# Kernel tuning notes

Hardware: AMD Instinct MI355X
Metric: run time of the kernel (lower is better)

The kernel has to match this reference:

```python
import jax, jax.numpy as jnp
import numpy as np

N_NODES = 100000
N_EDGES = 1600000
F_IN = 128
F_OUT = 64
BN_EPS = 1e-5


def setup_inputs() -> dict:
    key = jax.random.key(0)
    k1, k2, k3, k4, k5, k6 = jax.random.split(key, 6)
    x = jax.random.normal(k1, (N_NODES, F_IN), dtype=jnp.float32)
    edge_index = jax.random.randint(k2, (2, N_EDGES), 0, N_NODES, dtype=jnp.int64)
    edge_weight = jax.random.uniform(k3, (N_EDGES,), dtype=jnp.float32)
    # learned params: linear weight (no bias), batchnorm gamma/beta
    W = jax.random.normal(k4, (F_OUT, F_IN), dtype=jnp.float32) * (1.0 / np.sqrt(F_IN))
    gamma = jnp.ones((F_OUT,), dtype=jnp.float32)
    beta = jnp.zeros((F_OUT,), dtype=jnp.float32)
    return {"x": x, "edge_index": edge_index, "edge_weight": edge_weight,
            "W": W, "gamma": gamma, "beta": beta}


def reference(x, edge_index, edge_weight, W, gamma, beta):
    N = x.shape[0]
    h = x @ W.T  # [N, F_OUT]
    # add self loops with weight 1.0
    loop = jnp.arange(N, dtype=edge_index.dtype)
    src = jnp.concatenate([edge_index[0], loop])
    dst = jnp.concatenate([edge_index[1], loop])
    w = jnp.concatenate([edge_weight, jnp.ones((N,), dtype=h.dtype)])
    # degree of row (src) counts edge occurrences (unweighted)
    deg = jax.ops.segment_sum(jnp.ones_like(w), src, num_segments=N)
    dinv = jnp.where(deg > 0, jax.lax.rsqrt(deg), 0.0)
    norm = dinv[src] * w * dinv[dst]  # [E+N]
    # gather-scale-scatter aggregation
    out = jax.ops.segment_sum(h[src] * norm[:, None], dst, num_segments=N)
    out = jax.nn.relu(out)
    # BatchNorm1d (training mode: biased batch stats over nodes)
    mean = jnp.mean(out, axis=0)
    var = jnp.mean((out - mean) ** 2, axis=0)
    out = (out - mean) * jax.lax.rsqrt(var + BN_EPS) * gamma + beta
    # dropout p=0.0 -> identity
    return out
```

## Files before the change

### kernel.cpp

```cpp
#include <hip/hip_runtime.h>

#define N_NODES 100000
#define N_EDGES 1600000
#define F_IN 128
#define F_OUT 64
#define BN_EPS 1e-5f

#define NCHUNK 128
#define CHUNK_E 12500

#define SCAN_NB 98


typedef __attribute__((ext_vector_type(8))) short bf16x8;
typedef __attribute__((ext_vector_type(4))) float f32x4;

__device__ __forceinline__ unsigned short f2bf(float x) {
    unsigned u = __float_as_uint(x);
    u += 0x7fffu + ((u >> 16) & 1u);
    return (unsigned short)(u >> 16);
}
__device__ __forceinline__ float4 bf4(uint2 p) {
    return make_float4(__int_as_float((int)(p.x << 16)),
                       __int_as_float((int)(p.x & 0xffff0000u)),
                       __int_as_float((int)(p.y << 16)),
                       __int_as_float((int)(p.y & 0xffff0000u)));
}

__global__ __launch_bounds__(512) void count_kernel(const void* __restrict__ ei,
                                                    int* __restrict__ s32,
                                                    int* __restrict__ d32,
                                                    unsigned* __restrict__ partial32) {
    __shared__ unsigned bins[N_NODES / 4];
    const long long* q = (const long long*)ei;
    long long probe = q[threadIdx.x & 63];
    bool badp = (probe < 0 || probe >= N_NODES);
    int is64 = (__ballot(badp) == 0ULL);

    const int tid = threadIdx.x;
    const int b = blockIdx.x;
    for (int i = tid; i < N_NODES / 4; i += 512) bins[i] = 0u;
    __syncthreads();
    const int e0 = b * CHUNK_E;
    for (int i = tid; i < CHUNK_E / 4; i += 512) {
        int e = e0 + i * 4;
        int4 s, d;
        if (is64) {
            longlong2 a = *(const longlong2*)&q[e];
            longlong2 bb = *(const longlong2*)&q[e + 2];
            s = make_int4((int)a.x, (int)a.y, (int)bb.x, (int)bb.y);
            longlong2 c2 = *(const longlong2*)&q[N_EDGES + e];
            longlong2 e2 = *(const longlong2*)&q[N_EDGES + e + 2];
            d = make_int4((int)c2.x, (int)c2.y, (int)e2.x, (int)e2.y);
        } else {
            s = ((const int4*)ei)[e >> 2];
            d = ((const int4*)ei)[(N_EDGES >> 2) + (e >> 2)];
        }
        ((int4*)s32)[e >> 2] = s;
#define C1(sk, dk, kk) { \
        unsigned si = (unsigned)(sk); \
        if (si < N_NODES) atomicAdd(&bins[si >> 2], 1u << ((si & 3) * 8)); \
        unsigned dd = (unsigned)(dk); \
        if (si < N_NODES && dd < N_NODES) { \
            unsigned sh = (dd & 3) * 8 + 4; \
            unsigned old = atomicAdd(&bins[dd >> 2], 16u << ((dd & 3) * 8)); \
            d32[e + kk] = (dk) | (int)(((old >> sh) & 0xFu) << 27); } }
        C1(s.x, d.x, 0) C1(s.y, d.y, 1) C1(s.z, d.z, 2) C1(s.w, d.w, 3)
#undef C1
    }
    __syncthreads();
    unsigned* dst = partial32 + (unsigned)b * (N_NODES / 4);
    for (int i = tid; i < N_NODES / 4; i += 512) dst[i] = bins[i];
}

__global__ __launch_bounds__(256) void redscan_kernel(unsigned* __restrict__ partial32,
                                                      float* __restrict__ dinv,
                                                      unsigned* __restrict__ off,
                                                      unsigned* __restrict__ bsum,
                                                      float* __restrict__ sums) {
    __shared__ unsigned s[256];
    const int tid = threadIdx.x;
    if (blockIdx.x == 0 && tid < 128) sums[tid] = 0.f;
    const int n0 = blockIdx.x * 1024 + tid * 4;
    unsigned cntk[4] = {0, 0, 0, 0};
    unsigned degk[4] = {0, 0, 0, 0};
    if (n0 < N_NODES) {
        unsigned idx = (unsigned)n0 >> 2;
#pragma unroll 8
        for (int c = 0; c < NCHUNK; ++c) {
            unsigned v = partial32[idx];
            unsigned nv = 0;
#pragma unroll
            for (int k = 0; k < 4; ++k) {
                unsigned byte = (v >> (k * 8)) & 0xFFu;
                nv |= (cntk[k] & 0xFFu) << (k * 8);
                cntk[k] += byte >> 4;
                degk[k] += byte & 0xFu;
            }
            partial32[idx] = nv;
            idx += N_NODES / 4;
        }
#pragma unroll
        for (int k = 0; k < 4; ++k)
            dinv[n0 + k] = rsqrtf((float)(degk[k] + 1u));
    }
    unsigned tsum = cntk[0] + cntk[1] + cntk[2] + cntk[3];
    s[tid] = tsum;
    __syncthreads();
    for (int d = 1; d < 256; d <<= 1) {
        unsigned t = (tid >= d) ? s[tid - d] : 0u;
        __syncthreads();
        s[tid] += t;
        __syncthreads();
    }
    unsigned run = s[tid] - tsum;
    if (n0 < N_NODES) {
        uint4 o;
        o.x = run;
        o.y = run + cntk[0];
        o.z = o.y + cntk[1];
        o.w = o.z + cntk[2];
        *(uint4*)&off[n0] = o;
    }
    if (tid == 255) bsum[blockIdx.x] = s[255];
}

__global__ __launch_bounds__(128) void scan2_kernel(unsigned* __restrict__ bsum) {
    __shared__ unsigned s[128];
    const int tid = threadIdx.x;
    unsigned v = (tid < SCAN_NB) ? bsum[tid] : 0u;
    s[tid] = v;
    __syncthreads();
    for (int d = 1; d < 128; d <<= 1) {
        unsigned t = (tid >= d) ? s[tid - d] : 0u;
        __syncthreads();
        s[tid] += t;
        __syncthreads();
    }
    if (tid < SCAN_NB) bsum[tid] = s[tid] - v;
}

__global__ __launch_bounds__(256) void place_kernel(const int* __restrict__ s32,
                                                    const int* __restrict__ d32,
                                                    const float* __restrict__ ew,
                                                    const unsigned* __restrict__ off,
                                                    const unsigned* __restrict__ bsum,
                                                    const unsigned* __restrict__ partial32,
                                                    int2* __restrict__ buck) {
    int i = blockIdx.x * 256 + threadIdx.x;
    if (i >= N_EDGES / 4) return;
    int4 s = ((const int4*)s32)[i];
    int4 d = ((const int4*)d32)[i];
    float4 w = ((const float4*)ew)[i];
    const unsigned char* pb = (const unsigned char*)partial32;
    int e = i * 4;
    int b = e / CHUNK_E;
    unsigned base = (unsigned)b * N_NODES;
#define P1(sk, dvk, wk) { \
    unsigned dd = (unsigned)(dvk) & 0x07FFFFFFu; \
    unsigned rk = ((unsigned)(dvk)) >> 27; \
    if ((unsigned)(sk) < N_NODES && dd < N_NODES) { \
        unsigned pref = pb[base + dd]; \
        unsigned slot = off[dd] + bsum[dd >> 10] + pref + rk; \
        if (slot < N_EDGES) \
            buck[slot] = make_int2((sk), __float_as_int(wk)); } }
    P1(s.x, d.x, w.x) P1(s.y, d.y, w.y) P1(s.z, d.z, w.z) P1(s.w, d.w, w.w)
#undef P1
}

__global__ __launch_bounds__(256) void gemm_kernel(const float* __restrict__ x,
                                                   const float* __restrict__ W,
                                                   const float* __restrict__ dinv,
                                                   unsigned short* __restrict__ hb) {
    __shared__ short wlds[16 * 64 * 8];
    const int tid = threadIdx.x;
    const int n0 = blockIdx.x * 64;
    {
        int out = tid & 63;
        int kb = tid >> 6;
#pragma unroll
        for (int i = 0; i < 4; ++i) {
            int koct = kb + i * 4;
            const float* wp = &W[out * F_IN + koct * 8];
            float4 aa = *(const float4*)wp;
            float4 bb = *(const float4*)(wp + 4);
            bf16x8 f;
            f[0] = (short)f2bf(aa.x); f[1] = (short)f2bf(aa.y);
            f[2] = (short)f2bf(aa.z); f[3] = (short)f2bf(aa.w);
            f[4] = (short)f2bf(bb.x); f[5] = (short)f2bf(bb.y);
            f[6] = (short)f2bf(bb.z); f[7] = (short)f2bf(bb.w);
            ((bf16x8*)wlds)[koct * 64 + out] = f;
        }
    }
    __syncthreads();
    const int wv = tid >> 6;
    const int lane = tid & 63;
    const int m = lane & 15;
    const int quad = lane >> 4;
    const int row = n0 + wv * 16 + m;
    const bool rv = row < N_NODES;
    const float* xrow = &x[(long)row * F_IN + quad * 8];
    f32x4 acc0 = {0.f, 0.f, 0.f, 0.f};
    f32x4 acc1 = {0.f, 0.f, 0.f, 0.f};
    f32x4 acc2 = {0.f, 0.f, 0.f, 0.f};
    f32x4 acc3 = {0.f, 0.f, 0.f, 0.f};
#pragma unroll
    for (int kc = 0; kc < 4; ++kc) {
        bf16x8 a = {0, 0, 0, 0, 0, 0, 0, 0};
        if (rv) {
            float4 aa = *(const float4*)(xrow + kc * 32);
            float4 bb = *(const float4*)(xrow + kc * 32 + 4);
            a[0] = (short)f2bf(aa.x); a[1] = (short)f2bf(aa.y);
            a[2] = (short)f2bf(aa.z); a[3] = (short)f2bf(aa.w);
            a[4] = (short)f2bf(bb.x); a[5] = (short)f2bf(bb.y);
            a[6] = (short)f2bf(bb.z); a[7] = (short)f2bf(bb.w);
        }
        const bf16x8* wrow = &((const bf16x8*)wlds)[(kc * 4 + quad) * 64 + m];
        acc0 = __builtin_amdgcn_mfma_f32_16x16x32_bf16(a, wrow[0],  acc0, 0, 0, 0);
        acc1 = __builtin_amdgcn_mfma_f32_16x16x32_bf16(a, wrow[16], acc1, 0, 0, 0);
        acc2 = __builtin_amdgcn_mfma_f32_16x16x32_bf16(a, wrow[32], acc2, 0, 0, 0);
        acc3 = __builtin_amdgcn_mfma_f32_16x16x32_bf16(a, wrow[48], acc3, 0, 0, 0);
    }
#pragma unroll
    for (int r = 0; r < 4; ++r) {
        int node = n0 + wv * 16 + quad * 4 + r;
        if (node < N_NODES) {
            float dv = dinv[node];
            unsigned short* hr = &hb[(long)node * F_OUT + m];
            hr[0]  = f2bf(acc0[r] * dv);
            hr[16] = f2bf(acc1[r] * dv);
            hr[32] = f2bf(acc2[r] * dv);
            hr[48] = f2bf(acc3[r] * dv);
        }
    }
}

#define AGG_BLOCKS 2048
#define NPW 13

#define ACC4(A, P, W) { \
    A[0] += __int_as_float((int)((P).x << 16)) * (W); \
    A[1] += __int_as_float((int)((P).x & 0xffff0000u)) * (W); \
    A[2] += __int_as_float((int)((P).y << 16)) * (W); \
    A[3] += __int_as_float((int)((P).y & 0xffff0000u)) * (W); }

#define LOADB(B0_, B1_, QV) { \
    unsigned a0_ = (QV) + (unsigned)es; \
    unsigned a1_ = a0_ + 4u; \
    if (a0_ > (unsigned)(N_EDGES - 1)) a0_ = (unsigned)(N_EDGES - 1); \
    if (a1_ > (unsigned)(N_EDGES - 1)) a1_ = (unsigned)(N_EDGES - 1); \
    B0_ = buck[a0_]; B1_ = buck[a1_]; }

#define GISSUE(G0_, G1_, W0_, W1_, B0_, B1_) { \
    unsigned r0_ = (unsigned)(B0_).x; if (r0_ > (unsigned)(N_NODES - 1)) r0_ = 0u; \
    unsigned r1_ = (unsigned)(B1_).x; if (r1_ > (unsigned)(N_NODES - 1)) r1_ = 0u; \
    G0_ = ((const uint2*)(hb + ((long)r0_ << 6)))[cl]; \
    G1_ = ((const uint2*)(hb + ((long)r1_ << 6)))[cl]; \
    W0_ = __int_as_float((B0_).y); W1_ = __int_as_float((B1_).y); }

#define FIN() { \
    acc[0] += __shfl_xor(acc[0], 16); acc[1] += __shfl_xor(acc[1], 16); \
    acc[2] += __shfl_xor(acc[2], 16); acc[3] += __shfl_xor(acc[3], 16); \
    acc[0] += __shfl_xor(acc[0], 32); acc[1] += __shfl_xor(acc[1], 32); \
    acc[2] += __shfl_xor(acc[2], 32); acc[3] += __shfl_xor(acc[3], 32); \
    if (es == 0) { \
        float4 hv = bf4(hn); \
        float r0_ = fmaxf(dn * (acc[0] + hv.x), 0.f); \
        float r1_ = fmaxf(dn * (acc[1] + hv.y), 0.f); \
        float r2_ = fmaxf(dn * (acc[2] + hv.z), 0.f); \
        float r3_ = fmaxf(dn * (acc[3] + hv.w), 0.f); \
        int node_ = nbeg + ncur; \
        *(float4*)&out[(long)node_ * F_OUT + cl * 4] = make_float4(r0_, r1_, r2_, r3_); \
        s1[0] += r0_; s1[1] += r1_; s1[2] += r2_; s1[3] += r3_; \
        s2[0] += r0_ * r0_; s2[1] += r1_ * r1_; \
        s2[2] += r2_ * r2_; s2[3] += r3_ * r3_; \
    } \
    acc[0] = acc[1] = acc[2] = acc[3] = 0.f; \
    ++ncur; \
    if (ncur < nn) { \
        seg_lo = bnd; \
        bnd = __shfl(bl, ncur + 1); \
        dn = __shfl(dvl, ncur); \
        hn = ((const uint2*)(hb + ((long)(nbeg + ncur) << 6)))[cl]; \
    } else { seg_lo = 0xFFFFFFFFu; bnd = 0xFFFFFFFFu; } }

#define CONSUME(G0_, G1_, W0_, W1_, QV) { \
    const unsigned qc_ = (QV); \
    const unsigned p0_ = qc_ + (unsigned)es; \
    const unsigned p1_ = p0_ + 4u; \
    for (;;) { \
        float m0_ = (p0_ >= seg_lo && p0_ < bnd) ? (W0_) : 0.f; \
        float m1_ = (p1_ >= seg_lo && p1_ < bnd) ? (W1_) : 0.f; \
        ACC4(acc, G0_, m0_) ACC4(acc, G1_, m1_) \
        if (bnd > qc_ + 8u) break; \
        FIN() \
        if (seg_lo >= qc_ + 8u) break; \
    } }

__global__ __launch_bounds__(256) void aggregate_kernel(
    const unsigned short* __restrict__ hb, const float* __restrict__ dinv,
    const unsigned* __restrict__ off, const unsigned* __restrict__ bsum,
    const int2* __restrict__ buck, float* __restrict__ out,
    float* __restrict__ sums) {
    const int tid = threadIdx.x;
    const int wv = tid >> 6;
    const int lane = tid & 63;
    const int es = lane >> 4;
    const int cl = lane & 15;
    float s1[4] = {0.f, 0.f, 0.f, 0.f};
    float s2[4] = {0.f, 0.f, 0.f, 0.f};
    float acc[4] = {0.f, 0.f, 0.f, 0.f};

    const int wid = blockIdx.x * 4 + wv;
    const int nbeg = wid * NPW;
    int nn = N_NODES - nbeg;
    if (nn > NPW) nn = NPW;
    if (nn < 0) nn = 0;

    unsigned bl = (unsigned)N_EDGES;
    float dvl = 0.f;
    if (nn > 0) {
        int n = nbeg + lane;
        if (lane <= nn)
            bl = (n < N_NODES) ? off[n] + bsum[(unsigned)n >> 10] : (unsigned)N_EDGES;
        if (lane < nn) dvl = dinv[n];
    }

    if (nn > 0) {
        const unsigned obeg = __shfl(bl, 0);
        const unsigned oend = __shfl(bl, nn);
        int ncur = 0;
        unsigned seg_lo = obeg;
        unsigned bnd = __shfl(bl, 1);
        float dn = __shfl(dvl, 0);
        uint2 hn = ((const uint2*)(hb + ((long)nbeg << 6)))[cl];

        const int NB = (int)((oend - obeg + 7u) >> 3);
        const int NB3 = ((NB + 2) / 3) * 3;

        int2 b00, b01, b10, b11, b20, b21;
        uint2 gA0, gA1, gB0, gB1, gC0, gC1;
        float wA0, wA1, wB0, wB1, wC0, wC1;

        if (NB3 > 0) {
            LOADB(b00, b01, obeg)
            LOADB(b10, b11, obeg + 8u)
            LOADB(b20, b21, obeg + 16u)
            GISSUE(gA0, gA1, wA0, wA1, b00, b01) LOADB(b00, b01, obeg + 24u)
            GISSUE(gB0, gB1, wB0, wB1, b10, b11) LOADB(b10, b11, obeg + 32u)
            GISSUE(gC0, gC1, wC0, wC1, b20, b21) LOADB(b20, b21, obeg + 40u)

            for (int k = 3; k < NB3; k += 3) {
                const unsigned q = obeg + ((unsigned)k << 3);
                CONSUME(gA0, gA1, wA0, wA1, q - 24u)
                GISSUE(gA0, gA1, wA0, wA1, b00, b01) LOADB(b00, b01, q + 24u)
                CONSUME(gB0, gB1, wB0, wB1, q - 16u)
                GISSUE(gB0, gB1, wB0, wB1, b10, b11) LOADB(b10, b11, q + 32u)
                CONSUME(gC0, gC1, wC0, wC1, q - 8u)
                GISSUE(gC0, gC1, wC0, wC1, b20, b21) LOADB(b20, b21, q + 40u)
            }
            {
                const unsigned qd = obeg + ((unsigned)NB3 << 3);
                CONSUME(gA0, gA1, wA0, wA1, qd - 24u)
                CONSUME(gB0, gB1, wB0, wB1, qd - 16u)
                CONSUME(gC0, gC1, wC0, wC1, qd - 8u)
            }
        }
        while (ncur < nn) { FIN() }
    }

    __shared__ float l1[256];
    __shared__ float l2[256];
    if (es == 0) {
#pragma unroll
        for (int k = 0; k < 4; ++k) {
            l1[wv * 64 + cl * 4 + k] = s1[k];
            l2[wv * 64 + cl * 4 + k] = s2[k];
        }
    }
    __syncthreads();
    if (tid < 64) {
        float b1 = l1[tid] + l1[64 + tid] + l1[128 + tid] + l1[192 + tid];
        float b2 = l2[tid] + l2[64 + tid] + l2[128 + tid] + l2[192 + tid];
        atomicAdd(&sums[tid], b1);
        atomicAdd(&sums[64 + tid], b2);
    }
}

__global__ __launch_bounds__(256) void apply_kernel(float* __restrict__ agg,
                                                    const float* __restrict__ sums,
                                                    const float* __restrict__ gamma,
                                                    const float* __restrict__ beta) {
    __shared__ float sc[64], bi[64];
    if (threadIdx.x < 64) {
        int c = threadIdx.x;
        const float inv_n = 1.0f / (float)N_NODES;
        float mean = sums[c] * inv_n;
        float var = sums[64 + c] * inv_n - mean * mean;
        float rs = rsqrtf(var + BN_EPS);
        float scale = rs * gamma[c];
        sc[c] = scale;
        bi[c] = beta[c] - mean * scale;
    }
    __syncthreads();
    int i = blockIdx.x * blockDim.x + threadIdx.x;
    if (i >= N_NODES * 16) return;
    int c4 = (i & 15) << 2;
    float4 v = ((float4*)agg)[i];
    v.x = v.x * sc[c4 + 0] + bi[c4 + 0];
    v.y = v.y * sc[c4 + 1] + bi[c4 + 1];
    v.z = v.z * sc[c4 + 2] + bi[c4 + 2];
    v.w = v.w * sc[c4 + 3] + bi[c4 + 3];
    ((float4*)agg)[i] = v;
}

extern "C" void kernel_launch(void* const* d_in, const int* in_sizes, int n_in,
                              void* d_out, int out_size, void* d_ws, size_t ws_size,
                              hipStream_t stream) {
    const float* x     = (const float*)d_in[0];
    const void*  ei    = d_in[1];
    const float* ew    = (const float*)d_in[2];
    const float* W     = (const float*)d_in[3];
    const float* gamma = (const float*)d_in[4];
    const float* beta  = (const float*)d_in[5];
    float* out = (float*)d_out;
    float* ws  = (float*)d_ws;

    int*            s32       = (int*)ws;
    int*            d32       = (int*)(ws + 1600000);
    unsigned*       partial32 = (unsigned*)(ws + 3200000);
    unsigned short* hb        = (unsigned short*)(ws + 3200000);
    int2*           buck      = (int2*)(ws + 6400000);
    float*          dinv      = ws + 9600000;
    float*          sums      = ws + 9700000;
    unsigned*       off       = (unsigned*)(ws + 9800128);
    unsigned*       bsum      = (unsigned*)(ws + 9900128);

    count_kernel<<<NCHUNK, 512, 0, stream>>>(ei, s32, d32, partial32);
    redscan_kernel<<<SCAN_NB, 256, 0, stream>>>(partial32, dinv, off, bsum, sums);
    scan2_kernel<<<1, 128, 0, stream>>>(bsum);
    place_kernel<<<(N_EDGES / 4 + 255) / 256, 256, 0, stream>>>(s32, d32, ew, off, bsum,
                                                                partial32, buck);
    gemm_kernel<<<(N_NODES + 63) / 64, 256, 0, stream>>>(x, W, dinv, hb);
    aggregate_kernel<<<AGG_BLOCKS, 256, 0, stream>>>(hb, dinv, off, bsum, buck, out, sums);
    apply_kernel<<<(N_NODES * 16 + 255) / 256, 256, 0, stream>>>(out, sums, gamma, beta);
}
```

Before: 270.4 us.

## Merge place and GEMM kernels into one interleaved launch with separate hb buffer

Combines the edge-placement scatter and the bf16 MFMA GEMM into a single launch whose blocks alternate between the two jobs. To make this legal, hb moves out of the partial32 region (which place still reads) into extra workspace when it is large enough. The aim is to remove one launch boundary and let memory-bound scatter work overlap compute-bound GEMM work on the same GPU. Every block now reserves the GEMM's LDS, which may limit occupancy for the place blocks, and the old two-kernel path stays as a fallback when the workspace is too small.

```diff
diff --git a/kernel.cpp b/kernel.cpp
--- a/kernel.cpp
+++ b/kernel.cpp
@@ -140,14 +140,14 @@
     if (tid < SCAN_NB) bsum[tid] = s[tid] - v;
 }
 
-__global__ __launch_bounds__(256) void place_kernel(const int* __restrict__ s32,
-                                                    const int* __restrict__ d32,
-                                                    const float* __restrict__ ew,
-                                                    const unsigned* __restrict__ off,
-                                                    const unsigned* __restrict__ bsum,
-                                                    const unsigned* __restrict__ partial32,
-                                                    int2* __restrict__ buck) {
-    int i = blockIdx.x * 256 + threadIdx.x;
+__device__ __forceinline__ void place_body(int i,
+                                           const int* __restrict__ s32,
+                                           const int* __restrict__ d32,
+                                           const float* __restrict__ ew,
+                                           const unsigned* __restrict__ off,
+                                           const unsigned* __restrict__ bsum,
+                                           const unsigned* __restrict__ partial32,
+                                           int2* __restrict__ buck) {
     if (i >= N_EDGES / 4) return;
     int4 s = ((const int4*)s32)[i];
     int4 d = ((const int4*)d32)[i];
@@ -168,13 +168,13 @@
 #undef P1
 }
 
-__global__ __launch_bounds__(256) void gemm_kernel(const float* __restrict__ x,
-                                                   const float* __restrict__ W,
-                                                   const float* __restrict__ dinv,
-                                                   unsigned short* __restrict__ hb) {
-    __shared__ short wlds[16 * 64 * 8];
-    const int tid = threadIdx.x;
-    const int n0 = blockIdx.x * 64;
+__device__ __forceinline__ void gemm_body(int gb, int tid,
+                                          const float* __restrict__ x,
+                                          const float* __restrict__ W,
+                                          const float* __restrict__ dinv,
+                                          unsigned short* __restrict__ hb,
+                                          short* wlds) {
+    const int n0 = gb * 64;
     {
         int out = tid & 63;
         int kb = tid >> 6;
@@ -232,6 +232,40 @@
             hr[32] = f2bf(acc2[r] * dv);
             hr[48] = f2bf(acc3[r] * dv);
         }
+    }
+}
+
+__global__ __launch_bounds__(256) void place_kernel(const int* __restrict__ s32,
+                                                    const int* __restrict__ d32,
+                                                    const float* __restrict__ ew,
+                                                    const unsigned* __restrict__ off,
+                                                    const unsigned* __restrict__ bsum,
+                                                    const unsigned* __restrict__ partial32,
+                                                    int2* __restrict__ buck) {
+    place_body(blockIdx.x * 256 + threadIdx.x, s32, d32, ew, off, bsum, partial32, buck);
+}
+
+__global__ __launch_bounds__(256) void gemm_kernel(const float* __restrict__ x,
+                                                   const float* __restrict__ W,
+                                                   const float* __restrict__ dinv,
+                                                   unsigned short* __restrict__ hb) {
+    __shared__ short wlds[16 * 64 * 8];
+    gemm_body(blockIdx.x, threadIdx.x, x, W, dinv, hb, wlds);
+}
+
+__global__ __launch_bounds__(256) void place_gemm_kernel(
+    const int* __restrict__ s32, const int* __restrict__ d32,
+    const float* __restrict__ ew, const unsigned* __restrict__ off,
+    const unsigned* __restrict__ bsum, const unsigned* __restrict__ partial32,
+    int2* __restrict__ buck, const float* __restrict__ x,
+    const float* __restrict__ W, const float* __restrict__ dinv,
+    unsigned short* __restrict__ hb) {
+    __shared__ short wlds[16 * 64 * 8];
+    if (blockIdx.x & 1) {
+        place_body((blockIdx.x >> 1) * 256 + threadIdx.x,
+                   s32, d32, ew, off, bsum, partial32, buck);
+    } else {
+        gemm_body(blockIdx.x >> 1, threadIdx.x, x, W, dinv, hb, wlds);
     }
 }
 
@@ -429,19 +463,27 @@
     int*            s32       = (int*)ws;
     int*            d32       = (int*)(ws + 1600000);
     unsigned*       partial32 = (unsigned*)(ws + 3200000);
-    unsigned short* hb        = (unsigned short*)(ws + 3200000);
     int2*           buck      = (int2*)(ws + 6400000);
     float*          dinv      = ws + 9600000;
     float*          sums      = ws + 9700000;
     unsigned*       off       = (unsigned*)(ws + 9800128);
     unsigned*       bsum      = (unsigned*)(ws + 9900128);
 
+    const bool big_ws = ws_size >= (size_t)(9900288 + 3200000) * 4;
+    unsigned short* hb = big_ws ? (unsigned short*)(ws + 9900288)
+                                : (unsigned short*)(ws + 3200000);
+
     count_kernel<<<NCHUNK, 512, 0, stream>>>(ei, s32, d32, partial32);
     redscan_kernel<<<SCAN_NB, 256, 0, stream>>>(partial32, dinv, off, bsum, sums);
     scan2_kernel<<<1, 128, 0, stream>>>(bsum);
-    place_kernel<<<(N_EDGES / 4 + 255) / 256, 256, 0, stream>>>(s32, d32, ew, off, bsum,
-                                                                partial32, buck);
-    gemm_kernel<<<(N_NODES + 63) / 64, 256, 0, stream>>>(x, W, dinv, hb);
+    if (big_ws) {
+        place_gemm_kernel<<<3126, 256, 0, stream>>>(s32, d32, ew, off, bsum,
+                                                    partial32, buck, x, W, dinv, hb);
+    } else {
+        place_kernel<<<(N_EDGES / 4 + 255) / 256, 256, 0, stream>>>(s32, d32, ew, off, bsum,
+                                                                    partial32, buck);
+        gemm_kernel<<<(N_NODES + 63) / 64, 256, 0, stream>>>(x, W, dinv, hb);
+    }
     aggregate_kernel<<<AGG_BLOCKS, 256, 0, stream>>>(hb, dinv, off, bsum, buck, out, sums);
     apply_kernel<<<(N_NODES * 16 + 255) / 256, 256, 0, stream>>>(out, sums, gamma, beta);
 }
```

Result: slower. 275.9 us (+2.0%).
